# Kernel tuning notes

Hardware: AMD Instinct MI355X
Metric: run time of the kernel (lower is better)

Reference implementation:

```python
import jax, jax.numpy as jnp
import numpy as np

EPS = 1e-5

def layer_norm(x, g, b):
    mu = jnp.mean(x, axis=-1, keepdims=True)
    var = jnp.mean((x - mu) ** 2, axis=-1, keepdims=True)
    return (x - mu) * jax.lax.rsqrt(var + EPS) * g + b

def setup_inputs() -> dict:
    key = jax.random.key(0)
    ks = jax.random.split(key, 13)
    B, N, C, H = 2, 2048, 1024, 16
    Dff = 4 * C
    s = lambda k, shape, fan_in: jax.random.normal(k, shape, jnp.float32) * (1.0 / np.sqrt(fan_in))
    return {
        "x": jax.random.normal(ks[0], (B, N, C), jnp.float32),
        "ln1_g": jnp.ones((C,), jnp.float32),
        "ln1_b": jnp.zeros((C,), jnp.float32),
        "qkv_w": s(ks[1], (3 * C, C), C),
        "qkv_b": jnp.zeros((3 * C,), jnp.float32),
        "proj_w": s(ks[2], (C, C), C),
        "proj_b": jnp.zeros((C,), jnp.float32),
        "ln2_g": jnp.ones((C,), jnp.float32),
        "ln2_b": jnp.zeros((C,), jnp.float32),
        "fc1_w": s(ks[3], (Dff, C), C),
        "fc1_b": jnp.zeros((Dff,), jnp.float32),
        "fc2_w": s(ks[4], (C, Dff), Dff),
        "fc2_b": jnp.zeros((C,), jnp.float32),
    }

def reference(x, ln1_g, ln1_b, qkv_w, qkv_b, proj_w, proj_b, ln2_g, ln2_b, fc1_w, fc1_b, fc2_w, fc2_b):
    B, N, C = x.shape
    H = 16
    D = C // H
    # --- attention sub-block (pre-norm) ---
    h = layer_norm(x, ln1_g, ln1_b)
    qkv = h @ qkv_w.T + qkv_b                      # [B,N,3C]
    qkv = qkv.reshape(B, N, 3, H, D).transpose(2, 0, 3, 1, 4)  # [3,B,H,N,D]
    q, k, v = qkv[0], qkv[1], qkv[2]
    attn = jnp.einsum('bhnd,bhmd->bhnm', q, k) * (D ** -0.5)   # [B,H,N,N]
    attn = jax.nn.softmax(attn, axis=-1)
    o = jnp.einsum('bhnm,bhmd->bhnd', attn, v)     # [B,H,N,D]
    o = o.transpose(0, 2, 1, 3).reshape(B, N, C)
    x = x + (o @ proj_w.T + proj_b)
    # --- MLP sub-block (pre-norm) ---
    h = layer_norm(x, ln2_g, ln2_b)
    h = jax.nn.gelu(h @ fc1_w.T + fc1_b, approximate=False)
    x = x + (h @ fc2_w.T + fc2_b)
    return x
```

## Files before the change

kernel.cpp:

```cpp
#include <hip/hip_runtime.h>
#include <hip/hip_bf16.h>
#include <math.h>

typedef __bf16 bf16;
typedef __bf16 bf16x8 __attribute__((ext_vector_type(8)));
typedef __bf16 bf16x4 __attribute__((ext_vector_type(4)));
typedef float  f32x4  __attribute__((ext_vector_type(4)));

typedef __attribute__((address_space(1))) void gvoid;
typedef __attribute__((address_space(3))) void lvoid;
#define GLOAD_LDS16(gp, lp) __builtin_amdgcn_global_load_lds((gvoid*)(gp), (lvoid*)(lp), 16, 0, 0)

__global__ __launch_bounds__(256) void prep(
    const float* __restrict__ qkvw, const float* __restrict__ projw,
    const float* __restrict__ fc1w, const float* __restrict__ fc2w,
    bf16* __restrict__ qkvw_h, bf16* __restrict__ projw_h,
    bf16* __restrict__ fc1w_h, bf16* __restrict__ fc2w_h,
    const float* __restrict__ x, const float* __restrict__ g,
    const float* __restrict__ b, bf16* __restrict__ h1) {
  int blk = blockIdx.x;
  if (blk < 12288) {
    const float* in; bf16* out; int base;
    if (blk < 3072)      { in = qkvw; out = qkvw_h; base = blk; }
    else if (blk < 4096) { in = projw; out = projw_h; base = blk - 3072; }
    else if (blk < 8192) { in = fc1w; out = fc1w_h; base = blk - 4096; }
    else                 { in = fc2w; out = fc2w_h; base = blk - 8192; }
    int i = (base * 256 + threadIdx.x) * 4;
    f32x4 v = *(const f32x4*)(in + i);
    bf16x4 o;
    #pragma unroll
    for (int e = 0; e < 4; ++e) o[e] = (bf16)v[e];
    *(bf16x4*)(out + i) = o;
    return;
  }
  int w = threadIdx.x >> 6, l = threadIdx.x & 63;
  size_t row = (size_t)(blk - 12288) * 4 + w;
  const float* xr = x + row * 1024;
  float f[16];
  #pragma unroll
  for (int c = 0; c < 4; ++c) {
    f32x4 v = *(const f32x4*)(xr + c * 256 + l * 4);
    #pragma unroll
    for (int e = 0; e < 4; ++e) f[c * 4 + e] = v[e];
  }
  float s = 0.f, ss = 0.f;
  #pragma unroll
  for (int e = 0; e < 16; ++e) { s += f[e]; ss += f[e] * f[e]; }
  #pragma unroll
  for (int d = 1; d < 64; d <<= 1) { s += __shfl_xor(s, d); ss += __shfl_xor(ss, d); }
  float mean = s * (1.f / 1024.f);
  float var  = ss * (1.f / 1024.f) - mean * mean;
  float rstd = rsqrtf(var + 1e-5f);
  #pragma unroll
  for (int c = 0; c < 4; ++c) {
    f32x4 gv = *(const f32x4*)(g + c * 256 + l * 4);
    f32x4 bv = *(const f32x4*)(b + c * 256 + l * 4);
    bf16x4 ov;
    #pragma unroll
    for (int e = 0; e < 4; ++e)
      ov[e] = (bf16)((f[c * 4 + e] - mean) * rstd * gv[e] + bv[e]);
    *(bf16x4*)(h1 + row * 1024 + c * 256 + l * 4) = ov;
  }
}

__global__ __launch_bounds__(256) void ln_f32(const float* __restrict__ x,
    const float* __restrict__ g, const float* __restrict__ b, bf16* __restrict__ out) {
  int w = threadIdx.x >> 6, l = threadIdx.x & 63;
  size_t row = (size_t)blockIdx.x * 4 + w;
  const float* xr = x + row * 1024;
  float f[16];
  #pragma unroll
  for (int c = 0; c < 4; ++c) {
    f32x4 v = *(const f32x4*)(xr + c * 256 + l * 4);
    #pragma unroll
    for (int e = 0; e < 4; ++e) f[c * 4 + e] = v[e];
  }
  float s = 0.f, ss = 0.f;
  #pragma unroll
  for (int e = 0; e < 16; ++e) { s += f[e]; ss += f[e] * f[e]; }
  #pragma unroll
  for (int d = 1; d < 64; d <<= 1) { s += __shfl_xor(s, d); ss += __shfl_xor(ss, d); }
  float mean = s * (1.f / 1024.f);
  float var  = ss * (1.f / 1024.f) - mean * mean;
  float rstd = rsqrtf(var + 1e-5f);
  #pragma unroll
  for (int c = 0; c < 4; ++c) {
    f32x4 gv = *(const f32x4*)(g + c * 256 + l * 4);
    f32x4 bv = *(const f32x4*)(b + c * 256 + l * 4);
    bf16x4 ov;
    #pragma unroll
    for (int e = 0; e < 4; ++e)
      ov[e] = (bf16)((f[c * 4 + e] - mean) * rstd * gv[e] + bv[e]);
    *(bf16x4*)(out + row * 1024 + c * 256 + l * 4) = ov;
  }
}

#define SWZ(tp) ((tp) ^ ((((tp) >> 9) & 1) << 5))
#define STAGE(buf, op, half, kt_) do { \
    const char* gp_ = (const char*)((op) ? Wp : Ap); \
    int t0_ = (op) ? colBase : rowBase; \
    const int P_ = (op) ? 12 : 13; \
    _Pragma("unroll") for (int s_ = 0; s_ < 2; ++s_) { \
      int b14_ = w * 2048 + s_ * 1024; \
      int tb_ = ((b14_ >> P_) << (P_ + 1)) | ((half) << P_) | (b14_ & ((1 << P_) - 1)); \
      int tq_ = SWZ(tb_ + l * 16); \
      GLOAD_LDS16(gp_ + ((size_t)(t0_ + (tq_ >> 7)) * lda + (size_t)(kt_) * 64) * 2 + (tq_ & 127), \
                  smbase + (buf) * 65536 + (op) * 32768 + tb_); \
    } \
  } while (0)
#define LDA(buf, mi, kk) (*(const bf16x8*)(smbase + (buf) * 65536 + \
    SWZ((wm * 128 + (mi) * 16 + lr) * 128 + (kk) * 64 + lg * 16)))
#define LDB(buf, ni, kk) (*(const bf16x8*)(smbase + (buf) * 65536 + 32768 + \
    SWZ((wn * 64 + (ni) * 16 + lr) * 128 + (kk) * 64 + lg * 16)))
#define RD_A(buf, MI0) { _Pragma("unroll") for (int i_ = 0; i_ < 4; ++i_) \
    _Pragma("unroll") for (int k_ = 0; k_ < 2; ++k_) a[i_][k_] = LDA(buf, (MI0) + i_, k_); }
#define RD_B(buf, NI0) { _Pragma("unroll") for (int j_ = 0; j_ < 2; ++j_) \
    _Pragma("unroll") for (int k_ = 0; k_ < 2; ++k_) bq[j_][k_] = LDB(buf, (NI0) + j_, k_); }
#define MFMA16(MI0, NI0) do { __builtin_amdgcn_s_setprio(1); \
    _Pragma("unroll") for (int i_ = 0; i_ < 4; ++i_) \
    _Pragma("unroll") for (int j_ = 0; j_ < 2; ++j_) \
    _Pragma("unroll") for (int k_ = 0; k_ < 2; ++k_) \
      acc[(MI0) + i_][(NI0) + j_] = __builtin_amdgcn_mfma_f32_16x16x32_bf16( \
          a[i_][k_], bq[j_][k_], acc[(MI0) + i_][(NI0) + j_], 0, 0, 0); \
    __builtin_amdgcn_s_setprio(0); } while (0)
#define BARX() __builtin_amdgcn_s_barrier()
#define LGK0() asm volatile("s_waitcnt lgkmcnt(0)")
#define VM4()  asm volatile("s_waitcnt vmcnt(4)")

template<int ACT, int HASBIAS, typename TO>
__global__ __launch_bounds__(512, 2) void gemm256(const bf16* __restrict__ Ap,
    const bf16* __restrict__ Wp, const float* __restrict__ bias,
    TO* __restrict__ out, int lda, int N, int klen, int nbx, size_t outSlice) {
  __shared__ bf16 smem_[2][2][256 * 64];
  char* smbase = (char*)smem_;
  int tid = threadIdx.x, w = tid >> 6, l = tid & 63, lr = l & 15, lg = l >> 4;
  int wm = w >> 2, wn = w & 3;
  int q = gridDim.x >> 3;
  int wg = ((int)blockIdx.x & 7) * q + ((int)blockIdx.x >> 3);
  int rowBase = (wg / nbx) * 256, colBase = (wg % nbx) * 256;
  Ap += (size_t)blockIdx.y * klen;
  Wp += (size_t)blockIdx.y * klen;
  out += (size_t)blockIdx.y * outSlice;

  f32x4 acc[8][4];
  const f32x4 fz = {0.f, 0.f, 0.f, 0.f};
  #pragma unroll
  for (int i = 0; i < 8; ++i)
    #pragma unroll
    for (int j = 0; j < 4; ++j) acc[i][j] = fz;
  bf16x8 a[4][2], bq[2][2];
  int nkt = klen >> 6;

  STAGE(0, 0, 0, 0); STAGE(0, 1, 0, 0); STAGE(0, 0, 1, 0); STAGE(0, 1, 1, 0);
  STAGE(1, 1, 0, 1); STAGE(1, 0, 1, 1);
  VM4(); BARX();

  for (int t = 0; t < nkt; t += 2) {
    int t1 = t + 1;
    int t2 = t + 2 < nkt ? t + 2 : nkt - 1;
    int t3 = t + 3 < nkt ? t + 3 : nkt - 1;
    RD_A(0, 0); RD_B(0, 0);
    STAGE(1, 0, 0, t1); STAGE(1, 1, 1, t1);
    BARX(); LGK0(); MFMA16(0, 0); BARX();
    RD_A(0, 4);
    BARX(); LGK0(); MFMA16(4, 0); BARX();
    RD_B(0, 2);
    STAGE(0, 1, 0, t2);
    BARX(); LGK0(); MFMA16(4, 2); BARX();
    RD_A(0, 0);
    STAGE(0, 0, 1, t2);
    VM4();
    BARX(); LGK0(); MFMA16(0, 2); BARX();
    RD_A(1, 0); RD_B(1, 0);
    STAGE(0, 0, 0, t2); STAGE(0, 1, 1, t2);
    BARX(); LGK0(); MFMA16(0, 0); BARX();
    RD_A(1, 4);
    BARX(); LGK0(); MFMA16(4, 0); BARX();
    RD_B(1, 2);
    STAGE(1, 1, 0, t3);
    BARX(); LGK0(); MFMA16(4, 2); BARX();
    RD_A(1, 0);
    STAGE(1, 0, 1, t3);
    VM4();
    BARX(); LGK0(); MFMA16(0, 2); BARX();
  }

  #pragma unroll
  for (int ni = 0; ni < 4; ++ni) {
    int col = colBase + wn * 64 + ni * 16 + lr;
    float bv = HASBIAS ? bias[col] : 0.f;
    #pragma unroll
    for (int mi = 0; mi < 8; ++mi) {
      #pragma unroll
      for (int jj = 0; jj < 4; ++jj) {
        int row2 = rowBase + wm * 128 + mi * 16 + lg * 4 + jj;
        float v = acc[mi][ni][jj] + bv;
        if constexpr (ACT == 1) v = 0.5f * v * (1.f + erff(v * 0.70710678118f));
        out[(size_t)row2 * N + col] = (TO)v;
      }
    }
  }
}

__global__ __launch_bounds__(256) void fc2_red(const bf16* __restrict__ part,
    const float* __restrict__ x1, const float* __restrict__ bias,
    float* __restrict__ out) {
  int i = (blockIdx.x * 256 + threadIdx.x) * 4;
  f32x4 s = *(const f32x4*)(x1 + i);
  s += *(const f32x4*)(bias + (i & 1023));
  #pragma unroll
  for (int k = 0; k < 4; ++k) {
    bf16x4 pv = *(const bf16x4*)(part + (size_t)k * 4194304 + i);
    #pragma unroll
    for (int e = 0; e < 4; ++e) s[e] += (float)pv[e];
  }
  *(f32x4*)(out + i) = s;
}

template<int ACT, int HASRES, typename TO>
__global__ __launch_bounds__(256) void gemm_bt(const bf16* __restrict__ A,
    const bf16* __restrict__ W, const float* __restrict__ bias,
    const float* __restrict__ res, TO* __restrict__ out, int M, int N, int K) {
  __shared__ bf16 As[128 * 32];
  __shared__ bf16 Bs[128 * 32];
  int tid = threadIdx.x;
  int w = tid >> 6, l = tid & 63;
  int lr = l & 15, lg = l >> 4;
  int wm = w >> 1, wn = w & 1;
  int rowBase = blockIdx.y * 128;
  int colBase = blockIdx.x * 128;
  f32x4 acc[4][4];
  const f32x4 fz = {0.f, 0.f, 0.f, 0.f};
  #pragma unroll
  for (int i = 0; i < 4; ++i)
    #pragma unroll
    for (int j = 0; j < 4; ++j) acc[i][j] = fz;

  for (int kt = 0; kt < K; kt += 32) {
    __syncthreads();
    #pragma unroll
    for (int j = 0; j < 2; ++j) {
      int u = (w * 2 + j) * 64 + l;
      int r = u >> 2, cb = (u & 3) * 8;
      GLOAD_LDS16(A + (size_t)(rowBase + r) * K + kt + cb, As + (w * 2 + j) * 512);
      GLOAD_LDS16(W + (size_t)(colBase + r) * K + kt + cb, Bs + (w * 2 + j) * 512);
    }
    __syncthreads();
    bf16x8 af[4], bfr[4];
    #pragma unroll
    for (int mi = 0; mi < 4; ++mi)
      af[mi] = *(const bf16x8*)(As + (wm * 64 + mi * 16 + lr) * 32 + lg * 8);
    #pragma unroll
    for (int ni = 0; ni < 4; ++ni)
      bfr[ni] = *(const bf16x8*)(Bs + (wn * 64 + ni * 16 + lr) * 32 + lg * 8);
    #pragma unroll
    for (int mi = 0; mi < 4; ++mi)
      #pragma unroll
      for (int ni = 0; ni < 4; ++ni)
        acc[mi][ni] = __builtin_amdgcn_mfma_f32_16x16x32_bf16(af[mi], bfr[ni], acc[mi][ni], 0, 0, 0);
  }

  #pragma unroll
  for (int ni = 0; ni < 4; ++ni) {
    int col = colBase + wn * 64 + ni * 16 + lr;
    float bv = bias[col];
    #pragma unroll
    for (int mi = 0; mi < 4; ++mi) {
      #pragma unroll
      for (int jj = 0; jj < 4; ++jj) {
        int row2 = rowBase + wm * 64 + mi * 16 + lg * 4 + jj;
        float v = acc[mi][ni][jj] + bv;
        if constexpr (ACT == 1) v = 0.5f * v * (1.f + erff(v * 0.70710678118f));
        if constexpr (HASRES)   v += res[(size_t)row2 * N + col];
        out[(size_t)row2 * N + col] = (TO)v;
      }
    }
  }
}

__global__ __launch_bounds__(256) void attn_kernel(const bf16* __restrict__ qkv,
                                                   bf16* __restrict__ o) {
  const int Nn = 2048, C3 = 3072;
  int tid = threadIdx.x, w = tid >> 6, l = tid & 63, lr = l & 15, lg = l >> 4;
  int lin = blockIdx.x;
  int wg = (lin & 7) * 128 + (lin >> 3);
  int qb = wg & 31, bh = wg >> 5;
  int b = bh >> 4, h = bh & 15;
  size_t hb = (size_t)b * Nn * C3 + h * 64;
  const bf16* Qp = qkv + hb;
  __shared__ bf16 Ks[64 * 64];
  __shared__ bf16 Vt[64 * 72];
  __shared__ bf16 Ps[4][16 * 64];

  int q0 = qb * 64 + w * 16;
  bf16x8 qf[2];
  #pragma unroll
  for (int kk = 0; kk < 2; ++kk) {
    bf16x8 t = *(const bf16x8*)(Qp + (size_t)(q0 + lr) * C3 + kk * 32 + lg * 8);
    #pragma unroll
    for (int e = 0; e < 8; ++e) qf[kk][e] = (bf16)((float)t[e] * 0.18033688f);
  }

  int sz = (lr & 7) << 4;
  int kr0 = tid >> 3, c80 = (tid & 7) * 8;
  int kr1 = kr0 + 32;
  char* ksw0 = (char*)Ks + kr0 * 128 + ((c80 * 2) ^ ((kr0 & 7) << 4));
  char* ksw1 = (char*)Ks + kr1 * 128 + ((c80 * 2) ^ ((kr1 & 7) << 4));
  bf16* vtw0 = Vt + (w * 8) * 72 + l;
  bf16* vtw1 = Vt + (32 + w * 8) * 72 + l;
  const char* ksr0 = (const char*)Ks + lr * 128 + ((lg * 16) ^ sz);
  const char* ksr1 = (const char*)Ks + lr * 128 + ((64 + lg * 16) ^ sz);
  char* psb = (char*)Ps[w] + lr * 128;
  char* psw0 = psb + ((lg * 8) ^ sz);
  char* psw1 = psb + ((32 + lg * 8) ^ sz);
  char* psw2 = psb + ((64 + lg * 8) ^ sz);
  char* psw3 = psb + ((96 + lg * 8) ^ sz);
  const char* psr0 = psb + ((lg * 16) ^ sz);
  const char* psr1 = psb + ((64 + lg * 16) ^ sz);
  const bf16* vtr = Vt + lr * 72 + lg * 8;

  const bf16* kp0 = qkv + hb + 1024 + (size_t)kr0 * C3 + c80;
  const bf16* kp1 = qkv + hb + 1024 + (size_t)kr1 * C3 + c80;
  const bf16* vp0 = qkv + hb + 2048 + (size_t)l * C3 + w * 8;
  const bf16* vp1 = vp0 + 32;
  const int step = 64 * C3;

  const f32x4 fz = {0.f, 0.f, 0.f, 0.f};
  f32x4 oa[4];
  #pragma unroll
  for (int c = 0; c < 4; ++c) oa[c] = fz;
  float mrow = -1e30f, srow = 0.f;

  bf16x8 kreg0 = *(const bf16x8*)kp0; kp0 += step;
  bf16x8 kreg1 = *(const bf16x8*)kp1; kp1 += step;
  bf16x8 vreg0 = *(const bf16x8*)vp0; vp0 += step;
  bf16x8 vreg1 = *(const bf16x8*)vp1; vp1 += step;

  for (int t = 0; t < 32; ++t) {
    __syncthreads();
    *(bf16x8*)ksw0 = kreg0;
    *(bf16x8*)ksw1 = kreg1;
    #pragma unroll
    for (int e = 0; e < 8; ++e) vtw0[e * 72] = vreg0[e];
    #pragma unroll
    for (int e = 0; e < 8; ++e) vtw1[e * 72] = vreg1[e];
    __syncthreads();
    if (t < 31) {
      kreg0 = *(const bf16x8*)kp0; kp0 += step;
      kreg1 = *(const bf16x8*)kp1; kp1 += step;
      vreg0 = *(const bf16x8*)vp0; vp0 += step;
      vreg1 = *(const bf16x8*)vp1; vp1 += step;
    }

    f32x4 sc[4];
    __builtin_amdgcn_s_setprio(1);
    #pragma unroll
    for (int c = 0; c < 4; ++c) {
      f32x4 acm = fz;
      acm = __builtin_amdgcn_mfma_f32_16x16x32_bf16(
          *(const bf16x8*)(ksr0 + c * 2048), qf[0], acm, 0, 0, 0);
      acm = __builtin_amdgcn_mfma_f32_16x16x32_bf16(
          *(const bf16x8*)(ksr1 + c * 2048), qf[1], acm, 0, 0, 0);
      sc[c] = acm;
    }
    __builtin_amdgcn_s_setprio(0);

    float m0 = fmaxf(fmaxf(sc[0][0], sc[0][1]), fmaxf(sc[0][2], sc[0][3]));
    float m1 = fmaxf(fmaxf(sc[1][0], sc[1][1]), fmaxf(sc[1][2], sc[1][3]));
    float m2 = fmaxf(fmaxf(sc[2][0], sc[2][1]), fmaxf(sc[2][2], sc[2][3]));
    float m3 = fmaxf(fmaxf(sc[3][0], sc[3][1]), fmaxf(sc[3][2], sc[3][3]));
    float mt = fmaxf(fmaxf(m0, m1), fmaxf(m2, m3));
    mt = fmaxf(mt, __shfl_xor(mt, 16));
    mt = fmaxf(mt, __shfl_xor(mt, 32));
    if (!__all(mt - mrow <= 8.f)) {
      float mn = fmaxf(mrow, mt);
      float al = exp2f(mrow - mn);
      mrow = mn;
      srow *= al;
      #pragma unroll
      for (int c = 0; c < 4; ++c)
        #pragma unroll
        for (int j = 0; j < 4; ++j) oa[c][j] *= al;
    }
    float p[4][4];
    float rs = 0.f;
    #pragma unroll
    for (int c = 0; c < 4; ++c) {
      float r0 = exp2f(sc[c][0] - mrow), r1 = exp2f(sc[c][1] - mrow);
      float r2 = exp2f(sc[c][2] - mrow), r3 = exp2f(sc[c][3] - mrow);
      p[c][0] = r0; p[c][1] = r1; p[c][2] = r2; p[c][3] = r3;
      rs += (r0 + r1) + (r2 + r3);
    }
    rs += __shfl_xor(rs, 16);
    rs += __shfl_xor(rs, 32);
    srow += rs;

    bf16x4 pk0, pk1, pk2, pk3;
    #pragma unroll
    for (int j = 0; j < 4; ++j) {
      pk0[j] = (bf16)p[0][j]; pk1[j] = (bf16)p[1][j];
      pk2[j] = (bf16)p[2][j]; pk3[j] = (bf16)p[3][j];
    }
    *(bf16x4*)psw0 = pk0; *(bf16x4*)psw1 = pk1;
    *(bf16x4*)psw2 = pk2; *(bf16x4*)psw3 = pk3;
    bf16x8 pb0 = *(const bf16x8*)psr0;
    bf16x8 pb1 = *(const bf16x8*)psr1;
    __builtin_amdgcn_s_setprio(1);
    #pragma unroll
    for (int cd = 0; cd < 4; ++cd) {
      oa[cd] = __builtin_amdgcn_mfma_f32_16x16x32_bf16(
          *(const bf16x8*)(vtr + cd * 1152), pb0, oa[cd], 0, 0, 0);
      oa[cd] = __builtin_amdgcn_mfma_f32_16x16x32_bf16(
          *(const bf16x8*)(vtr + cd * 1152 + 32), pb1, oa[cd], 0, 0, 0);
    }
    __builtin_amdgcn_s_setprio(0);
  }

  float inv = 1.f / srow;
  size_t qr = (size_t)q0 + lr;
  #pragma unroll
  for (int cd = 0; cd < 4; ++cd)
    #pragma unroll
    for (int j = 0; j < 4; ++j)
      o[((size_t)b * Nn + qr) * 1024 + h * 64 + cd * 16 + lg * 4 + j] =
          (bf16)(oa[cd][j] * inv);
}

extern "C" void kernel_launch(void* const* d_in, const int* in_sizes, int n_in,
                              void* d_out, int out_size, void* d_ws, size_t ws_size,
                              hipStream_t stream) {
  (void)in_sizes; (void)n_in; (void)out_size;
  const float* x     = (const float*)d_in[0];
  const float* ln1g  = (const float*)d_in[1];
  const float* ln1b  = (const float*)d_in[2];
  const float* qkvw  = (const float*)d_in[3];
  const float* qkvb  = (const float*)d_in[4];
  const float* projw = (const float*)d_in[5];
  const float* projb = (const float*)d_in[6];
  const float* ln2g  = (const float*)d_in[7];
  const float* ln2b  = (const float*)d_in[8];
  const float* fc1w  = (const float*)d_in[9];
  const float* fc1b  = (const float*)d_in[10];
  const float* fc2w  = (const float*)d_in[11];
  const float* fc2b  = (const float*)d_in[12];

  char* ws = (char*)d_ws;
  bf16*  qkvw_h = (bf16*)(ws);
  bf16*  projw_h= (bf16*)(ws + (6ull  << 20));
  bf16*  fc1w_h = (bf16*)(ws + (8ull  << 20));
  bf16*  fc2w_h = (bf16*)(ws + (16ull << 20));
  bf16*  h1     = (bf16*)(ws + (24ull << 20));
  bf16*  qkv    = (bf16*)(ws + (32ull << 20));
  bf16*  ov     = (bf16*)(ws + (64ull << 20));
  float* x1     = (float*)(ws + (72ull << 20));
  bf16*  fc2p   = (bf16*)(ws + (96ull << 20));
  bf16*  h2  = h1;
  bf16*  ffn = qkv;
  bool big = ws_size >= (160ull << 20);

  const int M = 4096;
  prep<<<dim3(12288 + 1024), 256, 0, stream>>>(qkvw, projw, fc1w, fc2w,
      qkvw_h, projw_h, fc1w_h, fc2w_h, x, ln1g, ln1b, h1);
  gemm256<0, 1, bf16><<<dim3(192), dim3(512), 0, stream>>>(
      h1, qkvw_h, qkvb, qkv, 1024, 3072, 1024, 12, 0);
  attn_kernel<<<dim3(1024), 256, 0, stream>>>(qkv, ov);
  gemm_bt<0, 1, float><<<dim3(1024 / 128, M / 128), 256, 0, stream>>>(
      ov, projw_h, projb, x, x1, M, 1024, 1024);
  ln_f32<<<dim3(M / 4), 256, 0, stream>>>(x1, ln2g, ln2b, h2);
  gemm256<1, 1, bf16><<<dim3(256), dim3(512), 0, stream>>>(
      h2, fc1w_h, fc1b, ffn, 1024, 4096, 1024, 16, 0);
  if (big) {
    gemm256<0, 0, bf16><<<dim3(64, 4), dim3(512), 0, stream>>>(
        ffn, fc2w_h, nullptr, fc2p, 4096, 1024, 1024, 4, 4194304ull);
    fc2_red<<<dim3(4096), 256, 0, stream>>>(fc2p, x1, fc2b, (float*)d_out);
  } else {
    gemm_bt<0, 1, float><<<dim3(1024 / 128, M / 128), 256, 0, stream>>>(
        ffn, fc2w_h, fc2b, x1, (float*)d_out, M, 1024, 4096);
  }
}
```

Baseline: 279.3 us.

## Widen attention KV tile to 128 and split-K the projection GEMM with fused LN2

The attention kernel now stages 128 keys and values per iteration instead of 64, using a new swizzled transposed-V layout and two P·V half passes. This halves the number of barriers and loop iterations and amortises softmax bookkeeping over more keys, at the cost of more LDS and registers. Separately, when the workspace is large, the output projection uses the 256-tile split-K GEMM into bf16 partials. A new kernel then reduces those partials, adds the residual and bias, and applies LayerNorm 2 in one pass, replacing the separate gemm_bt and ln_f32 launches.

```diff
diff --git a/kernel.cpp b/kernel.cpp
--- a/kernel.cpp
+++ b/kernel.cpp
@@ -202,6 +202,50 @@
   }
 }
 
+__global__ __launch_bounds__(256) void projred_ln(const bf16* __restrict__ part,
+    const float* __restrict__ x, const float* __restrict__ pb,
+    const float* __restrict__ g, const float* __restrict__ bb,
+    float* __restrict__ x1, bf16* __restrict__ h2) {
+  int w = threadIdx.x >> 6, l = threadIdx.x & 63;
+  size_t row = (size_t)blockIdx.x * 4 + w;
+  size_t rb = row * 1024;
+  float f[16];
+  #pragma unroll
+  for (int c = 0; c < 4; ++c) {
+    int off = c * 256 + l * 4;
+    f32x4 v = *(const f32x4*)(x + rb + off);
+    v += *(const f32x4*)(pb + off);
+    #pragma unroll
+    for (int sl = 0; sl < 4; ++sl) {
+      bf16x4 pv = *(const bf16x4*)(part + (size_t)sl * 4194304 + rb + off);
+      #pragma unroll
+      for (int e = 0; e < 4; ++e) v[e] += (float)pv[e];
+    }
+    *(f32x4*)(x1 + rb + off) = v;
+    #pragma unroll
+    for (int e = 0; e < 4; ++e) f[c * 4 + e] = v[e];
+  }
+  float s = 0.f, ss = 0.f;
+  #pragma unroll
+  for (int e = 0; e < 16; ++e) { s += f[e]; ss += f[e] * f[e]; }
+  #pragma unroll
+  for (int d = 1; d < 64; d <<= 1) { s += __shfl_xor(s, d); ss += __shfl_xor(ss, d); }
+  float mean = s * (1.f / 1024.f);
+  float var  = ss * (1.f / 1024.f) - mean * mean;
+  float rstd = rsqrtf(var + 1e-5f);
+  #pragma unroll
+  for (int c = 0; c < 4; ++c) {
+    int off = c * 256 + l * 4;
+    f32x4 gv = *(const f32x4*)(g + off);
+    f32x4 bv = *(const f32x4*)(bb + off);
+    bf16x4 ov;
+    #pragma unroll
+    for (int e = 0; e < 4; ++e)
+      ov[e] = (bf16)((f[c * 4 + e] - mean) * rstd * gv[e] + bv[e]);
+    *(bf16x4*)(h2 + rb + off) = ov;
+  }
+}
+
 __global__ __launch_bounds__(256) void fc2_red(const bf16* __restrict__ part,
     const float* __restrict__ x1, const float* __restrict__ bias,
     float* __restrict__ out) {
@@ -235,7 +279,6 @@
   for (int i = 0; i < 4; ++i)
     #pragma unroll
     for (int j = 0; j < 4; ++j) acc[i][j] = fz;
-
   for (int kt = 0; kt < K; kt += 32) {
     __syncthreads();
     #pragma unroll
@@ -259,7 +302,6 @@
       for (int ni = 0; ni < 4; ++ni)
         acc[mi][ni] = __builtin_amdgcn_mfma_f32_16x16x32_bf16(af[mi], bfr[ni], acc[mi][ni], 0, 0, 0);
   }
-
   #pragma unroll
   for (int ni = 0; ni < 4; ++ni) {
     int col = colBase + wn * 64 + ni * 16 + lr;
@@ -288,8 +330,8 @@
   int b = bh >> 4, h = bh & 15;
   size_t hb = (size_t)b * Nn * C3 + h * 64;
   const bf16* Qp = qkv + hb;
-  __shared__ bf16 Ks[64 * 64];
-  __shared__ bf16 Vt[64 * 72];
+  __shared__ bf16 Ks[128 * 64];
+  __shared__ bf16 Vt[64 * 128];
   __shared__ bf16 Ps[4][16 * 64];
 
   int q0 = qb * 64 + w * 16;
@@ -302,14 +344,16 @@
   }
 
   int sz = (lr & 7) << 4;
-  int kr0 = tid >> 3, c80 = (tid & 7) * 8;
-  int kr1 = kr0 + 32;
-  char* ksw0 = (char*)Ks + kr0 * 128 + ((c80 * 2) ^ ((kr0 & 7) << 4));
-  char* ksw1 = (char*)Ks + kr1 * 128 + ((c80 * 2) ^ ((kr1 & 7) << 4));
-  bf16* vtw0 = Vt + (w * 8) * 72 + l;
-  bf16* vtw1 = Vt + (32 + w * 8) * 72 + l;
+  int kr = tid >> 3, c80 = (tid & 7) * 8;
+  char* ksw = (char*)Ks + kr * 128 + ((c80 * 2) ^ ((kr & 7) << 4));
   const char* ksr0 = (const char*)Ks + lr * 128 + ((lg * 16) ^ sz);
   const char* ksr1 = (const char*)Ks + lr * 128 + ((64 + lg * 16) ^ sz);
+  char* vtw = (char*)Vt + w * 2048;
+  int l2 = l * 2;
+  int Bv = lr * 256 + ((lg * 16) ^ ((lr & 3) << 4));
+  int sw6 = (lr & 4) << 4;
+  const char* vtrA = (const char*)Vt + Bv + sw6;
+  const char* vtrB = (const char*)Vt + Bv + (64 ^ sw6);
   char* psb = (char*)Ps[w] + lr * 128;
   char* psw0 = psb + ((lg * 8) ^ sz);
   char* psw1 = psb + ((32 + lg * 8) ^ sz);
@@ -317,13 +361,14 @@
   char* psw3 = psb + ((96 + lg * 8) ^ sz);
   const char* psr0 = psb + ((lg * 16) ^ sz);
   const char* psr1 = psb + ((64 + lg * 16) ^ sz);
-  const bf16* vtr = Vt + lr * 72 + lg * 8;
-
-  const bf16* kp0 = qkv + hb + 1024 + (size_t)kr0 * C3 + c80;
-  const bf16* kp1 = qkv + hb + 1024 + (size_t)kr1 * C3 + c80;
+
+  const bf16* kp0 = qkv + hb + 1024 + (size_t)kr * C3 + c80;
+  const bf16* kp1 = kp0 + (size_t)32 * C3;
+  const bf16* kp2 = kp0 + (size_t)64 * C3;
+  const bf16* kp3 = kp0 + (size_t)96 * C3;
   const bf16* vp0 = qkv + hb + 2048 + (size_t)l * C3 + w * 8;
-  const bf16* vp1 = vp0 + 32;
-  const int step = 64 * C3;
+  const bf16* vp2 = vp0 + (size_t)64 * C3;
+  const int step = 128 * C3;
 
   const f32x4 fz = {0.f, 0.f, 0.f, 0.f};
   f32x4 oa[4];
@@ -331,31 +376,45 @@
   for (int c = 0; c < 4; ++c) oa[c] = fz;
   float mrow = -1e30f, srow = 0.f;
 
-  bf16x8 kreg0 = *(const bf16x8*)kp0; kp0 += step;
-  bf16x8 kreg1 = *(const bf16x8*)kp1; kp1 += step;
-  bf16x8 vreg0 = *(const bf16x8*)vp0; vp0 += step;
-  bf16x8 vreg1 = *(const bf16x8*)vp1; vp1 += step;
-
-  for (int t = 0; t < 32; ++t) {
+  bf16x8 kg0 = *(const bf16x8*)kp0; kp0 += step;
+  bf16x8 kg1 = *(const bf16x8*)kp1; kp1 += step;
+  bf16x8 kg2 = *(const bf16x8*)kp2; kp2 += step;
+  bf16x8 kg3 = *(const bf16x8*)kp3; kp3 += step;
+  bf16x8 vg0 = *(const bf16x8*)vp0;
+  bf16x8 vg1 = *(const bf16x8*)(vp0 + 32); vp0 += step;
+  bf16x8 vg2 = *(const bf16x8*)vp2;
+  bf16x8 vg3 = *(const bf16x8*)(vp2 + 32); vp2 += step;
+
+  for (int t = 0; t < 16; ++t) {
     __syncthreads();
-    *(bf16x8*)ksw0 = kreg0;
-    *(bf16x8*)ksw1 = kreg1;
-    #pragma unroll
-    for (int e = 0; e < 8; ++e) vtw0[e * 72] = vreg0[e];
-    #pragma unroll
-    for (int e = 0; e < 8; ++e) vtw1[e * 72] = vreg1[e];
+    *(bf16x8*)(ksw)         = kg0;
+    *(bf16x8*)(ksw + 4096)  = kg1;
+    *(bf16x8*)(ksw + 8192)  = kg2;
+    *(bf16x8*)(ksw + 12288) = kg3;
+    #pragma unroll
+    for (int e = 0; e < 8; ++e) {
+      int kx = l2 ^ (e << 4);
+      *(bf16*)(vtw + e * 256 + kx)              = vg0[e];
+      *(bf16*)(vtw + 8192 + e * 256 + kx)       = vg1[e];
+      *(bf16*)(vtw + e * 256 + kx + 128)        = vg2[e];
+      *(bf16*)(vtw + 8192 + e * 256 + kx + 128) = vg3[e];
+    }
     __syncthreads();
-    if (t < 31) {
-      kreg0 = *(const bf16x8*)kp0; kp0 += step;
-      kreg1 = *(const bf16x8*)kp1; kp1 += step;
-      vreg0 = *(const bf16x8*)vp0; vp0 += step;
-      vreg1 = *(const bf16x8*)vp1; vp1 += step;
-    }
-
-    f32x4 sc[4];
+    if (t < 15) {
+      kg0 = *(const bf16x8*)kp0; kp0 += step;
+      kg1 = *(const bf16x8*)kp1; kp1 += step;
+      kg2 = *(const bf16x8*)kp2; kp2 += step;
+      kg3 = *(const bf16x8*)kp3; kp3 += step;
+      vg0 = *(const bf16x8*)vp0;
+      vg1 = *(const bf16x8*)(vp0 + 32); vp0 += step;
+      vg2 = *(const bf16x8*)vp2;
+      vg3 = *(const bf16x8*)(vp2 + 32); vp2 += step;
+    }
+
+    f32x4 sc[8];
     __builtin_amdgcn_s_setprio(1);
     #pragma unroll
-    for (int c = 0; c < 4; ++c) {
+    for (int c = 0; c < 8; ++c) {
       f32x4 acm = fz;
       acm = __builtin_amdgcn_mfma_f32_16x16x32_bf16(
           *(const bf16x8*)(ksr0 + c * 2048), qf[0], acm, 0, 0, 0);
@@ -365,11 +424,12 @@
     }
     __builtin_amdgcn_s_setprio(0);
 
-    float m0 = fmaxf(fmaxf(sc[0][0], sc[0][1]), fmaxf(sc[0][2], sc[0][3]));
-    float m1 = fmaxf(fmaxf(sc[1][0], sc[1][1]), fmaxf(sc[1][2], sc[1][3]));
-    float m2 = fmaxf(fmaxf(sc[2][0], sc[2][1]), fmaxf(sc[2][2], sc[2][3]));
-    float m3 = fmaxf(fmaxf(sc[3][0], sc[3][1]), fmaxf(sc[3][2], sc[3][3]));
-    float mt = fmaxf(fmaxf(m0, m1), fmaxf(m2, m3));
+    float mv[8];
+    #pragma unroll
+    for (int c = 0; c < 8; ++c)
+      mv[c] = fmaxf(fmaxf(sc[c][0], sc[c][1]), fmaxf(sc[c][2], sc[c][3]));
+    float mt = fmaxf(fmaxf(fmaxf(mv[0], mv[1]), fmaxf(mv[2], mv[3])),
+                     fmaxf(fmaxf(mv[4], mv[5]), fmaxf(mv[6], mv[7])));
     mt = fmaxf(mt, __shfl_xor(mt, 16));
     mt = fmaxf(mt, __shfl_xor(mt, 32));
     if (!__all(mt - mrow <= 8.f)) {
@@ -382,38 +442,39 @@
         #pragma unroll
         for (int j = 0; j < 4; ++j) oa[c][j] *= al;
     }
-    float p[4][4];
     float rs = 0.f;
     #pragma unroll
-    for (int c = 0; c < 4; ++c) {
-      float r0 = exp2f(sc[c][0] - mrow), r1 = exp2f(sc[c][1] - mrow);
-      float r2 = exp2f(sc[c][2] - mrow), r3 = exp2f(sc[c][3] - mrow);
-      p[c][0] = r0; p[c][1] = r1; p[c][2] = r2; p[c][3] = r3;
-      rs += (r0 + r1) + (r2 + r3);
+    for (int c = 0; c < 8; ++c) {
+      #pragma unroll
+      for (int j = 0; j < 4; ++j) { sc[c][j] = exp2f(sc[c][j] - mrow); }
+      rs += (sc[c][0] + sc[c][1]) + (sc[c][2] + sc[c][3]);
     }
     rs += __shfl_xor(rs, 16);
     rs += __shfl_xor(rs, 32);
     srow += rs;
 
-    bf16x4 pk0, pk1, pk2, pk3;
-    #pragma unroll
-    for (int j = 0; j < 4; ++j) {
-      pk0[j] = (bf16)p[0][j]; pk1[j] = (bf16)p[1][j];
-      pk2[j] = (bf16)p[2][j]; pk3[j] = (bf16)p[3][j];
-    }
-    *(bf16x4*)psw0 = pk0; *(bf16x4*)psw1 = pk1;
-    *(bf16x4*)psw2 = pk2; *(bf16x4*)psw3 = pk3;
-    bf16x8 pb0 = *(const bf16x8*)psr0;
-    bf16x8 pb1 = *(const bf16x8*)psr1;
-    __builtin_amdgcn_s_setprio(1);
-    #pragma unroll
-    for (int cd = 0; cd < 4; ++cd) {
-      oa[cd] = __builtin_amdgcn_mfma_f32_16x16x32_bf16(
-          *(const bf16x8*)(vtr + cd * 1152), pb0, oa[cd], 0, 0, 0);
-      oa[cd] = __builtin_amdgcn_mfma_f32_16x16x32_bf16(
-          *(const bf16x8*)(vtr + cd * 1152 + 32), pb1, oa[cd], 0, 0, 0);
-    }
-    __builtin_amdgcn_s_setprio(0);
+#define PVHALF(HF) do { \
+      bf16x4 pk0, pk1, pk2, pk3; \
+      _Pragma("unroll") for (int j = 0; j < 4; ++j) { \
+        pk0[j] = (bf16)sc[(HF) * 4 + 0][j]; pk1[j] = (bf16)sc[(HF) * 4 + 1][j]; \
+        pk2[j] = (bf16)sc[(HF) * 4 + 2][j]; pk3[j] = (bf16)sc[(HF) * 4 + 3][j]; \
+      } \
+      *(bf16x4*)psw0 = pk0; *(bf16x4*)psw1 = pk1; \
+      *(bf16x4*)psw2 = pk2; *(bf16x4*)psw3 = pk3; \
+      bf16x8 pb0 = *(const bf16x8*)psr0; \
+      bf16x8 pb1 = *(const bf16x8*)psr1; \
+      __builtin_amdgcn_s_setprio(1); \
+      _Pragma("unroll") for (int cd = 0; cd < 4; ++cd) { \
+        oa[cd] = __builtin_amdgcn_mfma_f32_16x16x32_bf16( \
+            *(const bf16x8*)(vtrA + cd * 4096 + (HF) * 128), pb0, oa[cd], 0, 0, 0); \
+        oa[cd] = __builtin_amdgcn_mfma_f32_16x16x32_bf16( \
+            *(const bf16x8*)(vtrB + cd * 4096 + (HF) * 128), pb1, oa[cd], 0, 0, 0); \
+      } \
+      __builtin_amdgcn_s_setprio(0); \
+    } while (0)
+    PVHALF(0);
+    PVHALF(1);
+#undef PVHALF
   }
 
   float inv = 1.f / srow;
@@ -453,7 +514,7 @@
   bf16*  qkv    = (bf16*)(ws + (32ull << 20));
   bf16*  ov     = (bf16*)(ws + (64ull << 20));
   float* x1     = (float*)(ws + (72ull << 20));
-  bf16*  fc2p   = (bf16*)(ws + (96ull << 20));
+  bf16*  parts  = (bf16*)(ws + (96ull << 20));
   bf16*  h2  = h1;
   bf16*  ffn = qkv;
   bool big = ws_size >= (160ull << 20);
@@ -464,17 +525,23 @@
   gemm256<0, 1, bf16><<<dim3(192), dim3(512), 0, stream>>>(
       h1, qkvw_h, qkvb, qkv, 1024, 3072, 1024, 12, 0);
   attn_kernel<<<dim3(1024), 256, 0, stream>>>(qkv, ov);
-  gemm_bt<0, 1, float><<<dim3(1024 / 128, M / 128), 256, 0, stream>>>(
-      ov, projw_h, projb, x, x1, M, 1024, 1024);
-  ln_f32<<<dim3(M / 4), 256, 0, stream>>>(x1, ln2g, ln2b, h2);
+  if (big) {
+    gemm256<0, 0, bf16><<<dim3(64, 4), dim3(512), 0, stream>>>(
+        ov, projw_h, nullptr, parts, 1024, 1024, 256, 4, 4194304ull);
+    projred_ln<<<dim3(1024), 256, 0, stream>>>(parts, x, projb, ln2g, ln2b, x1, h2);
+  } else {
+    gemm_bt<0, 1, float><<<dim3(8, 32), 256, 0, stream>>>(
+        ov, projw_h, projb, x, x1, M, 1024, 1024);
+    ln_f32<<<dim3(1024), 256, 0, stream>>>(x1, ln2g, ln2b, h2);
+  }
   gemm256<1, 1, bf16><<<dim3(256), dim3(512), 0, stream>>>(
       h2, fc1w_h, fc1b, ffn, 1024, 4096, 1024, 16, 0);
   if (big) {
     gemm256<0, 0, bf16><<<dim3(64, 4), dim3(512), 0, stream>>>(
-        ffn, fc2w_h, nullptr, fc2p, 4096, 1024, 1024, 4, 4194304ull);
-    fc2_red<<<dim3(4096), 256, 0, stream>>>(fc2p, x1, fc2b, (float*)d_out);
+        ffn, fc2w_h, nullptr, parts, 4096, 1024, 1024, 4, 4194304ull);
+    fc2_red<<<dim3(4096), 256, 0, stream>>>(parts, x1, fc2b, (float*)d_out);
   } else {
-    gemm_bt<0, 1, float><<<dim3(1024 / 128, M / 128), 256, 0, stream>>>(
+    gemm_bt<0, 1, float><<<dim3(8, 32), 256, 0, stream>>>(
         ffn, fc2w_h, fc2b, x1, (float*)d_out, M, 1024, 4096);
   }
 }
```

Result: slower. 286.6 us (+2.6%).

## Double-buffer attention K/V tiles and split-K proj GEMM fused with LN2

Applied to the files above, without the earlier changes.

The attention kernel now keeps two K/V tiles in LDS, writing the next tile after the PV MFMAs and syncing once per iteration instead of twice. The V transpose now uses an XOR-swizzled layout in place of the padded one. When the workspace is large, the projection GEMM runs as a split-K gemm256 that writes bf16 partials, and a new kernel sums the partials with the residual and bias and applies LayerNorm 2 in one pass. The aim is less barrier stall in attention and better GPU occupancy for the small proj GEMM, at the cost of more LDS per block and extra partial-buffer traffic with bf16 rounding of the partials.

```diff
diff --git a/kernel.cpp b/kernel.cpp
--- a/kernel.cpp
+++ b/kernel.cpp
@@ -202,6 +202,50 @@
   }
 }
 
+__global__ __launch_bounds__(256) void projred_ln(const bf16* __restrict__ part,
+    const float* __restrict__ x, const float* __restrict__ pb,
+    const float* __restrict__ g, const float* __restrict__ bb,
+    float* __restrict__ x1, bf16* __restrict__ h2) {
+  int w = threadIdx.x >> 6, l = threadIdx.x & 63;
+  size_t row = (size_t)blockIdx.x * 4 + w;
+  size_t rb = row * 1024;
+  float f[16];
+  #pragma unroll
+  for (int c = 0; c < 4; ++c) {
+    int off = c * 256 + l * 4;
+    f32x4 v = *(const f32x4*)(x + rb + off);
+    v += *(const f32x4*)(pb + off);
+    #pragma unroll
+    for (int sl = 0; sl < 4; ++sl) {
+      bf16x4 pv = *(const bf16x4*)(part + (size_t)sl * 4194304 + rb + off);
+      #pragma unroll
+      for (int e = 0; e < 4; ++e) v[e] += (float)pv[e];
+    }
+    *(f32x4*)(x1 + rb + off) = v;
+    #pragma unroll
+    for (int e = 0; e < 4; ++e) f[c * 4 + e] = v[e];
+  }
+  float s = 0.f, ss = 0.f;
+  #pragma unroll
+  for (int e = 0; e < 16; ++e) { s += f[e]; ss += f[e] * f[e]; }
+  #pragma unroll
+  for (int d = 1; d < 64; d <<= 1) { s += __shfl_xor(s, d); ss += __shfl_xor(ss, d); }
+  float mean = s * (1.f / 1024.f);
+  float var  = ss * (1.f / 1024.f) - mean * mean;
+  float rstd = rsqrtf(var + 1e-5f);
+  #pragma unroll
+  for (int c = 0; c < 4; ++c) {
+    int off = c * 256 + l * 4;
+    f32x4 gv = *(const f32x4*)(g + off);
+    f32x4 bv = *(const f32x4*)(bb + off);
+    bf16x4 ov;
+    #pragma unroll
+    for (int e = 0; e < 4; ++e)
+      ov[e] = (bf16)((f[c * 4 + e] - mean) * rstd * gv[e] + bv[e]);
+    *(bf16x4*)(h2 + rb + off) = ov;
+  }
+}
+
 __global__ __launch_bounds__(256) void fc2_red(const bf16* __restrict__ part,
     const float* __restrict__ x1, const float* __restrict__ bias,
     float* __restrict__ out) {
@@ -235,7 +279,6 @@
   for (int i = 0; i < 4; ++i)
     #pragma unroll
     for (int j = 0; j < 4; ++j) acc[i][j] = fz;
-
   for (int kt = 0; kt < K; kt += 32) {
     __syncthreads();
     #pragma unroll
@@ -259,7 +302,6 @@
       for (int ni = 0; ni < 4; ++ni)
         acc[mi][ni] = __builtin_amdgcn_mfma_f32_16x16x32_bf16(af[mi], bfr[ni], acc[mi][ni], 0, 0, 0);
   }
-
   #pragma unroll
   for (int ni = 0; ni < 4; ++ni) {
     int col = colBase + wn * 64 + ni * 16 + lr;
@@ -288,8 +330,8 @@
   int b = bh >> 4, h = bh & 15;
   size_t hb = (size_t)b * Nn * C3 + h * 64;
   const bf16* Qp = qkv + hb;
-  __shared__ bf16 Ks[64 * 64];
-  __shared__ bf16 Vt[64 * 72];
+  __shared__ bf16 Ks[2][64 * 64];
+  __shared__ bf16 Vt[2][64 * 64];
   __shared__ bf16 Ps[4][16 * 64];
 
   int q0 = qb * 64 + w * 16;
@@ -302,14 +344,15 @@
   }
 
   int sz = (lr & 7) << 4;
+  int s45 = (lr & 3) << 4, s6 = (lr & 4) << 4;
+  int l2 = l * 2;
   int kr0 = tid >> 3, c80 = (tid & 7) * 8;
-  int kr1 = kr0 + 32;
-  char* ksw0 = (char*)Ks + kr0 * 128 + ((c80 * 2) ^ ((kr0 & 7) << 4));
-  char* ksw1 = (char*)Ks + kr1 * 128 + ((c80 * 2) ^ ((kr1 & 7) << 4));
-  bf16* vtw0 = Vt + (w * 8) * 72 + l;
-  bf16* vtw1 = Vt + (32 + w * 8) * 72 + l;
+  char* ksw = (char*)Ks + kr0 * 128 + ((c80 * 2) ^ ((kr0 & 7) << 4));
+  char* vtw = (char*)Vt + w * 1024;
   const char* ksr0 = (const char*)Ks + lr * 128 + ((lg * 16) ^ sz);
-  const char* ksr1 = (const char*)Ks + lr * 128 + ((64 + lg * 16) ^ sz);
+  const char* ksr1 = (const char*)Ks + lr * 128 + (((64) + lg * 16) ^ sz);
+  const char* vtrA = (const char*)Vt + lr * 128 + ((lg * 16) ^ s45) + s6;
+  const char* vtrB = (const char*)Vt + lr * 128 + ((lg * 16) ^ s45) + (64 ^ s6);
   char* psb = (char*)Ps[w] + lr * 128;
   char* psw0 = psb + ((lg * 8) ^ sz);
   char* psw1 = psb + ((32 + lg * 8) ^ sz);
@@ -317,12 +360,10 @@
   char* psw3 = psb + ((96 + lg * 8) ^ sz);
   const char* psr0 = psb + ((lg * 16) ^ sz);
   const char* psr1 = psb + ((64 + lg * 16) ^ sz);
-  const bf16* vtr = Vt + lr * 72 + lg * 8;
 
   const bf16* kp0 = qkv + hb + 1024 + (size_t)kr0 * C3 + c80;
-  const bf16* kp1 = qkv + hb + 1024 + (size_t)kr1 * C3 + c80;
+  const bf16* kp1 = kp0 + (size_t)32 * C3;
   const bf16* vp0 = qkv + hb + 2048 + (size_t)l * C3 + w * 8;
-  const bf16* vp1 = vp0 + 32;
   const int step = 64 * C3;
 
   const f32x4 fz = {0.f, 0.f, 0.f, 0.f};
@@ -331,25 +372,26 @@
   for (int c = 0; c < 4; ++c) oa[c] = fz;
   float mrow = -1e30f, srow = 0.f;
 
-  bf16x8 kreg0 = *(const bf16x8*)kp0; kp0 += step;
-  bf16x8 kreg1 = *(const bf16x8*)kp1; kp1 += step;
-  bf16x8 vreg0 = *(const bf16x8*)vp0; vp0 += step;
-  bf16x8 vreg1 = *(const bf16x8*)vp1; vp1 += step;
+  bf16x8 kg0 = *(const bf16x8*)kp0; kp0 += step;
+  bf16x8 kg1 = *(const bf16x8*)kp1; kp1 += step;
+  bf16x8 vg0 = *(const bf16x8*)vp0;
+  bf16x8 vg1 = *(const bf16x8*)(vp0 + 32); vp0 += step;
+  *(bf16x8*)(ksw) = kg0;
+  *(bf16x8*)(ksw + 4096) = kg1;
+  #pragma unroll
+  for (int e = 0; e < 8; ++e) {
+    *(bf16*)(vtw + e * 128 + (l2 ^ (e << 4)))        = vg0[e];
+    *(bf16*)(vtw + 4096 + e * 128 + (l2 ^ (e << 4))) = vg1[e];
+  }
+  __syncthreads();
 
   for (int t = 0; t < 32; ++t) {
-    __syncthreads();
-    *(bf16x8*)ksw0 = kreg0;
-    *(bf16x8*)ksw1 = kreg1;
-    #pragma unroll
-    for (int e = 0; e < 8; ++e) vtw0[e * 72] = vreg0[e];
-    #pragma unroll
-    for (int e = 0; e < 8; ++e) vtw1[e * 72] = vreg1[e];
-    __syncthreads();
+    int bo = (t & 1) << 13;
     if (t < 31) {
-      kreg0 = *(const bf16x8*)kp0; kp0 += step;
-      kreg1 = *(const bf16x8*)kp1; kp1 += step;
-      vreg0 = *(const bf16x8*)vp0; vp0 += step;
-      vreg1 = *(const bf16x8*)vp1; vp1 += step;
+      kg0 = *(const bf16x8*)kp0; kp0 += step;
+      kg1 = *(const bf16x8*)kp1; kp1 += step;
+      vg0 = *(const bf16x8*)vp0;
+      vg1 = *(const bf16x8*)(vp0 + 32); vp0 += step;
     }
 
     f32x4 sc[4];
@@ -358,9 +400,9 @@
     for (int c = 0; c < 4; ++c) {
       f32x4 acm = fz;
       acm = __builtin_amdgcn_mfma_f32_16x16x32_bf16(
-          *(const bf16x8*)(ksr0 + c * 2048), qf[0], acm, 0, 0, 0);
+          *(const bf16x8*)(ksr0 + bo + c * 2048), qf[0], acm, 0, 0, 0);
       acm = __builtin_amdgcn_mfma_f32_16x16x32_bf16(
-          *(const bf16x8*)(ksr1 + c * 2048), qf[1], acm, 0, 0, 0);
+          *(const bf16x8*)(ksr1 + bo + c * 2048), qf[1], acm, 0, 0, 0);
       sc[c] = acm;
     }
     __builtin_amdgcn_s_setprio(0);
@@ -409,11 +451,23 @@
     #pragma unroll
     for (int cd = 0; cd < 4; ++cd) {
       oa[cd] = __builtin_amdgcn_mfma_f32_16x16x32_bf16(
-          *(const bf16x8*)(vtr + cd * 1152), pb0, oa[cd], 0, 0, 0);
+          *(const bf16x8*)(vtrA + bo + cd * 2048), pb0, oa[cd], 0, 0, 0);
       oa[cd] = __builtin_amdgcn_mfma_f32_16x16x32_bf16(
-          *(const bf16x8*)(vtr + cd * 1152 + 32), pb1, oa[cd], 0, 0, 0);
+          *(const bf16x8*)(vtrB + bo + cd * 2048), pb1, oa[cd], 0, 0, 0);
     }
     __builtin_amdgcn_s_setprio(0);
+
+    if (t < 31) {
+      int bo2 = bo ^ 8192;
+      *(bf16x8*)(ksw + bo2) = kg0;
+      *(bf16x8*)(ksw + 4096 + bo2) = kg1;
+      #pragma unroll
+      for (int e = 0; e < 8; ++e) {
+        *(bf16*)(vtw + bo2 + e * 128 + (l2 ^ (e << 4)))        = vg0[e];
+        *(bf16*)(vtw + bo2 + 4096 + e * 128 + (l2 ^ (e << 4))) = vg1[e];
+      }
+      __syncthreads();
+    }
   }
 
   float inv = 1.f / srow;
@@ -453,7 +507,7 @@
   bf16*  qkv    = (bf16*)(ws + (32ull << 20));
   bf16*  ov     = (bf16*)(ws + (64ull << 20));
   float* x1     = (float*)(ws + (72ull << 20));
-  bf16*  fc2p   = (bf16*)(ws + (96ull << 20));
+  bf16*  parts  = (bf16*)(ws + (96ull << 20));
   bf16*  h2  = h1;
   bf16*  ffn = qkv;
   bool big = ws_size >= (160ull << 20);
@@ -464,17 +518,23 @@
   gemm256<0, 1, bf16><<<dim3(192), dim3(512), 0, stream>>>(
       h1, qkvw_h, qkvb, qkv, 1024, 3072, 1024, 12, 0);
   attn_kernel<<<dim3(1024), 256, 0, stream>>>(qkv, ov);
-  gemm_bt<0, 1, float><<<dim3(1024 / 128, M / 128), 256, 0, stream>>>(
-      ov, projw_h, projb, x, x1, M, 1024, 1024);
-  ln_f32<<<dim3(M / 4), 256, 0, stream>>>(x1, ln2g, ln2b, h2);
+  if (big) {
+    gemm256<0, 0, bf16><<<dim3(64, 4), dim3(512), 0, stream>>>(
+        ov, projw_h, nullptr, parts, 1024, 1024, 256, 4, 4194304ull);
+    projred_ln<<<dim3(1024), 256, 0, stream>>>(parts, x, projb, ln2g, ln2b, x1, h2);
+  } else {
+    gemm_bt<0, 1, float><<<dim3(8, 32), 256, 0, stream>>>(
+        ov, projw_h, projb, x, x1, M, 1024, 1024);
+    ln_f32<<<dim3(1024), 256, 0, stream>>>(x1, ln2g, ln2b, h2);
+  }
   gemm256<1, 1, bf16><<<dim3(256), dim3(512), 0, stream>>>(
       h2, fc1w_h, fc1b, ffn, 1024, 4096, 1024, 16, 0);
   if (big) {
     gemm256<0, 0, bf16><<<dim3(64, 4), dim3(512), 0, stream>>>(
-        ffn, fc2w_h, nullptr, fc2p, 4096, 1024, 1024, 4, 4194304ull);
-    fc2_red<<<dim3(4096), 256, 0, stream>>>(fc2p, x1, fc2b, (float*)d_out);
+        ffn, fc2w_h, nullptr, parts, 4096, 1024, 1024, 4, 4194304ull);
+    fc2_red<<<dim3(4096), 256, 0, stream>>>(parts, x1, fc2b, (float*)d_out);
   } else {
-    gemm_bt<0, 1, float><<<dim3(1024 / 128, M / 128), 256, 0, stream>>>(
+    gemm_bt<0, 1, float><<<dim3(8, 32), 256, 0, stream>>>(
         ffn, fc2w_h, fc2b, x1, (float*)d_out, M, 1024, 4096);
   }
 }
```

Measured after the change: 281.0 us. About the same (+0.6%).
